# Performance work log

Hardware: AMD Instinct MI355X
Metric: run time of the kernel (lower is better)

## Reference

```python
import jax, jax.numpy as jnp
import numpy as np

N_NODES = 100000
N_EDGES = 3200000
IN_DIM = 256
HID = 16
OUT = 10


def setup_inputs() -> dict:
    key = jax.random.key(0)
    k1, k2, k3, k4, k5, k6 = jax.random.split(key, 6)
    x = jax.random.normal(k1, (N_NODES, IN_DIM), dtype=jnp.float32)
    edge_index = jax.random.randint(k2, (2, N_EDGES), 0, N_NODES, dtype=jnp.int64)
    # Glorot-style init for GCN weights, zeros for bias (PyG defaults)
    W1 = jax.random.normal(k3, (IN_DIM, HID), dtype=jnp.float32) * (1.0 / np.sqrt(IN_DIM))
    b1 = jnp.zeros((HID,), dtype=jnp.float32)
    W2 = jax.random.normal(k4, (HID, OUT), dtype=jnp.float32) * (1.0 / np.sqrt(HID))
    b2 = jnp.zeros((OUT,), dtype=jnp.float32)
    return {"x": x, "edge_index": edge_index, "W1": W1, "b1": b1, "W2": W2, "b2": b2}


def _gcn_conv(h, src, dst, W, b, num_nodes):
    # GCNConv(normalize=False): out_i = sum_{(j->i) in E} (h_j W) + b
    m = h @ W                                   # [N, F_out] small GEMM
    agg = jax.ops.segment_sum(m[src], dst, num_segments=num_nodes)  # gather+scatter-add
    return agg + b


def reference(x, edge_index, W1, b1, W2, b2):
    src = edge_index[0]  # message source (flow: source_to_target)
    dst = edge_index[1]
    n = x.shape[0]
    h = jax.nn.relu(_gcn_conv(x, src, dst, W1, b1, n))
    # F.dropout with module in eval mode -> identity
    out = _gcn_conv(h, src, dst, W2, b2, n)
    return out
```

## Files before the change

### kernel.cpp

```cpp
#include <hip/hip_runtime.h>
#include <hip/hip_bf16.h>
#include <stdint.h>

#define IN_DIM 256
#define HID 16
#define OUTD 10
#define BKT_SHIFT 8
#define BKT_W 256
#define PART_CH 2048
#define EPT 8

typedef short v8s __attribute__((ext_vector_type(8)));
typedef float v4f __attribute__((ext_vector_type(4)));

__device__ __forceinline__ float bf2f(unsigned short u) {
    return __uint_as_float(((unsigned int)u) << 16);
}
__device__ __forceinline__ unsigned short f2bf(float f) {
    unsigned int u = __float_as_uint(f);
    unsigned int lsb = (u >> 16) & 1u;
    u += 0x7fffu + lsb;
    return (unsigned short)(u >> 16);
}

__device__ __forceinline__ int load_dst(const void* ei, int n_edges, int e, int is64) {
    return is64 ? (int)((const long long*)ei)[(size_t)n_edges + e]
                : ((const int*)ei)[(size_t)n_edges + e];
}
__device__ __forceinline__ int load_src(const void* ei, int n_edges, int e, int is64) {
    return is64 ? (int)((const long long*)ei)[e] : ((const int*)ei)[e];
}

__global__ void setup_w1_kernel(const void* __restrict__ x,
                                const void* __restrict__ W1,
                                const void* __restrict__ ei,
                                int n_nodes, int* __restrict__ flags,
                                int* __restrict__ bucket_cnt, int K,
                                unsigned short* __restrict__ W1split) {
    int b = blockIdx.x, t = threadIdx.x;
    int gid = b * blockDim.x + t;
    for (int i = gid; i < K; i += gridDim.x * blockDim.x) bucket_cnt[i] = 0;

    if (b == 16) {
        if (t < 64) {
            const unsigned short* xs = (const unsigned short*)x;
            const unsigned short* ws = (const unsigned short*)W1;
            bool badx = false, badw = false;
#pragma unroll
            for (int q = 0; q < 4; ++q) {
                float vx = bf2f(xs[t + 64 * q]);
                float vw = bf2f(ws[t + 64 * q]);
                if (!(vx > -1e4f && vx < 1e4f)) badx = true;
                if (!(vw > -1e4f && vw < 1e4f)) badw = true;
            }
            const unsigned long long* e64 = (const unsigned long long*)ei;
            bool big = false;
#pragma unroll
            for (int q = 0; q < 2; ++q)
                if (e64[t + 64 * q] >= (unsigned long long)n_nodes) big = true;
            int xf32 = __any(badx) ? 1 : 0;
            int wf32 = __any(badw) ? 1 : 0;
            int is64 = __any(big) ? 0 : 1;
            if (t == 0) { flags[0] = is64; flags[1] = xf32; flags[2] = wf32; }
        }
        return;
    }

    __shared__ int swf32;
    if (t == 0) swf32 = 0;
    __syncthreads();
    {
        float vw = bf2f(((const unsigned short*)W1)[t]);
        if (!(vw > -1e4f && vw < 1e4f)) swf32 = 1;
    }
    __syncthreads();
    const int wf32 = swf32;

    int i = b * 256 + t;
    float w = wf32 ? ((const float*)W1)[i]
                   : bf2f(((const unsigned short*)W1)[i]);
    unsigned short hi = f2bf(w);
    unsigned short lo = f2bf(w - bf2f(hi));
    int k = i >> 4, n = i & 15;
    int kk = k >> 5, qd = (k >> 3) & 3, j = k & 7;
    int idx = ((kk * 4 + qd) * 16 + n) * 8 + j;
    W1split[idx] = hi;
    W1split[4096 + idx] = lo;
}

__global__ __launch_bounds__(256, 4) void gemm1_bhist_kernel(
        const void* __restrict__ xp_,
        const unsigned short* __restrict__ W1split,
        unsigned short* __restrict__ m1,
        const void* __restrict__ ei,
        int* __restrict__ bucket_cnt,
        int n_nodes, int n_edges, int K,
        const int* __restrict__ flags, int g_gemm) {
    __shared__ int lh[512];
    int t = threadIdx.x;
    if ((int)blockIdx.x >= g_gemm) {
        for (int i = t; i < 512; i += 256) lh[i] = 0;
        __syncthreads();
        int is64 = flags[0];
        int vbid = blockIdx.x - g_gemm;
        int stride = (gridDim.x - g_gemm) * 256;
        for (int e = vbid * 256 + t; e < n_edges; e += stride) {
            int d = load_dst(ei, n_edges, e, is64);
            atomicAdd(&lh[d >> BKT_SHIFT], 1);
        }
        __syncthreads();
        for (int i = t; i < K; i += 256)
            if (lh[i]) atomicAdd(&bucket_cnt[i], lh[i]);
        return;
    }
    const int xf32 = flags[1];
    int lane = t & 63;
    int wave = t >> 6;
    int col  = lane & 15;
    int quad = lane >> 4;
    int n_tiles = (n_nodes + 15) >> 4;
    const unsigned short* Whi = W1split;
    const unsigned short* Wlo = W1split + 4096;

    if (!xf32) {
        const unsigned short* x = (const unsigned short*)xp_;
        for (int tile = blockIdx.x * 4 + wave; tile < n_tiles; tile += g_gemm * 4) {
            int row = tile * 16 + col;
            int r = row < n_nodes ? row : n_nodes - 1;
            const unsigned short* xp = x + (size_t)r * IN_DIM + quad * 8;
            v8s a[8];
#pragma unroll
            for (int kk = 0; kk < 8; ++kk)
                a[kk] = *(const v8s*)(xp + kk * 32);
            v4f acc1 = {0.f, 0.f, 0.f, 0.f};
            v4f acc2 = {0.f, 0.f, 0.f, 0.f};
#pragma unroll
            for (int kk = 0; kk < 8; ++kk) {
                v8s bh = *(const v8s*)&Whi[(kk * 64 + lane) * 8];
                v8s bl = *(const v8s*)&Wlo[(kk * 64 + lane) * 8];
                acc1 = __builtin_amdgcn_mfma_f32_16x16x32_bf16(a[kk], bh, acc1, 0, 0, 0);
                acc2 = __builtin_amdgcn_mfma_f32_16x16x32_bf16(a[kk], bl, acc2, 0, 0, 0);
            }
#pragma unroll
            for (int rg = 0; rg < 4; ++rg) {
                int node = tile * 16 + quad * 4 + rg;
                if (node < n_nodes)
                    m1[(size_t)node * HID + col] = f2bf(acc1[rg] + acc2[rg]);
            }
        }
    } else {
        const float* x = (const float*)xp_;
        for (int tile = blockIdx.x * 4 + wave; tile < n_tiles; tile += g_gemm * 4) {
            int row = tile * 16 + col;
            int r = row < n_nodes ? row : n_nodes - 1;
            const float* xp = x + (size_t)r * IN_DIM + quad * 8;
            float4 u[16];
#pragma unroll
            for (int kk = 0; kk < 8; ++kk) {
                u[2 * kk]     = *(const float4*)(xp + kk * 32);
                u[2 * kk + 1] = *(const float4*)(xp + kk * 32 + 4);
            }
            v4f acc1 = {0.f, 0.f, 0.f, 0.f};
            v4f acc2 = {0.f, 0.f, 0.f, 0.f};
#pragma unroll
            for (int kk = 0; kk < 8; ++kk) {
                float uv[8] = {u[2 * kk].x,     u[2 * kk].y,
                               u[2 * kk].z,     u[2 * kk].w,
                               u[2 * kk + 1].x, u[2 * kk + 1].y,
                               u[2 * kk + 1].z, u[2 * kk + 1].w};
                v8s ahi, alo;
#pragma unroll
                for (int j = 0; j < 8; ++j) {
                    unsigned short hi = f2bf(uv[j]);
                    unsigned short lo = f2bf(uv[j] - bf2f(hi));
                    ahi[j] = (short)hi; alo[j] = (short)lo;
                }
                v8s bh = *(const v8s*)&Whi[(kk * 64 + lane) * 8];
                v8s bl = *(const v8s*)&Wlo[(kk * 64 + lane) * 8];
                acc1 = __builtin_amdgcn_mfma_f32_16x16x32_bf16(ahi, bh, acc1, 0, 0, 0);
                acc2 = __builtin_amdgcn_mfma_f32_16x16x32_bf16(ahi, bl, acc2, 0, 0, 0);
                acc2 = __builtin_amdgcn_mfma_f32_16x16x32_bf16(alo, bh, acc2, 0, 0, 0);
            }
#pragma unroll
            for (int rg = 0; rg < 4; ++rg) {
                int node = tile * 16 + quad * 4 + rg;
                if (node < n_nodes)
                    m1[(size_t)node * HID + col] = f2bf(acc1[rg] + acc2[rg]);
            }
        }
    }
}

__global__ void bscan_kernel(const int* __restrict__ bucket_cnt, int K,
                             int* __restrict__ bucket_off, int* __restrict__ bcur,
                             int* __restrict__ row_off, int n_nodes, int n_edges) {
    __shared__ int ts[256];
    int t = threadIdx.x;
    const int KP = (K + 255) / 256;
    int base = t * KP;
    int local[8];
    int s = 0;
    for (int q = 0; q < KP; ++q) {
        int idx = base + q;
        int v = (idx < K) ? bucket_cnt[idx] : 0;
        local[q] = v; s += v;
    }
    ts[t] = s;
    __syncthreads();
    for (int off = 1; off < 256; off <<= 1) {
        int v = (t >= off) ? ts[t - off] : 0;
        __syncthreads();
        ts[t] += v;
        __syncthreads();
    }
    int ex = ts[t] - s;
    for (int q = 0; q < KP; ++q) {
        int idx = base + q;
        if (idx < K) { bucket_off[idx] = ex; bcur[idx] = ex; }
        ex += local[q];
    }
    if (t == 255) bucket_off[K] = ex;
    if (t == 0) row_off[n_nodes] = n_edges;
}

__global__ void part_kernel(const void* __restrict__ ei, int n_edges,
                            int* __restrict__ bcur, unsigned int* __restrict__ pairs,
                            const int* __restrict__ flags, int K) {
    __shared__ int lh[512];
    __shared__ int gdelta[512];
    __shared__ int ts[256];
    __shared__ unsigned int spairs[PART_CH];
    __shared__ unsigned short sbkt[PART_CH];
    int begin = blockIdx.x * PART_CH;
    int is64 = flags[0];
    int t = threadIdx.x;
    lh[t] = 0; lh[t + 256] = 0;

    int dloc[EPT];
#pragma unroll
    for (int i = 0; i < EPT; ++i) {
        int e = begin + i * 256 + t;
        dloc[i] = (e < n_edges) ? load_dst(ei, n_edges, e, is64) : -1;
    }
    __syncthreads();
#pragma unroll
    for (int i = 0; i < EPT; ++i)
        if (dloc[i] >= 0) atomicAdd(&lh[dloc[i] >> BKT_SHIFT], 1);
    __syncthreads();

    int c0 = lh[2 * t], c1 = lh[2 * t + 1];
    int s = c0 + c1;
    ts[t] = s;
    __syncthreads();
    for (int off = 1; off < 256; off <<= 1) {
        int v = (t >= off) ? ts[t - off] : 0;
        __syncthreads();
        ts[t] += v;
        __syncthreads();
    }
    int ex = ts[t] - s;
    if (c0 > 0) gdelta[2 * t]     = atomicAdd(&bcur[2 * t], c0) - ex;
    if (c1 > 0) gdelta[2 * t + 1] = atomicAdd(&bcur[2 * t + 1], c1) - (ex + c0);
    __syncthreads();
    lh[2 * t] = ex; lh[2 * t + 1] = ex + c0;
    __syncthreads();

#pragma unroll
    for (int i = 0; i < EPT; ++i) {
        int e = begin + i * 256 + t;
        if (dloc[i] >= 0) {
            int srcv = load_src(ei, n_edges, e, is64);
            int b = dloc[i] >> BKT_SHIFT;
            int lpos = atomicAdd(&lh[b], 1);
            spairs[lpos] = ((unsigned)srcv << 8) | ((unsigned)dloc[i] & (BKT_W - 1));
            sbkt[lpos] = (unsigned short)b;
        }
    }
    __syncthreads();

    int total = n_edges - begin; if (total > PART_CH) total = PART_CH;
    for (int j = t; j < total; j += 256)
        pairs[gdelta[sbkt[j]] + j] = spairs[j];
}

__global__ void csr_kernel(const unsigned int* __restrict__ pairs,
                           const int* __restrict__ bucket_off,
                           int* __restrict__ row_off, int* __restrict__ csr_src,
                           int n_nodes) {
    __shared__ int deg[BKT_W];
    __shared__ int cur[BKT_W];
    __shared__ int ts[BKT_W];
    int blk = blockIdx.x;
    int nbase = blk << BKT_SHIFT;
    int NL = n_nodes - nbase; if (NL > BKT_W) NL = BKT_W;
    int beg = bucket_off[blk], end = bucket_off[blk + 1];
    int t = threadIdx.x;
    if (t < BKT_W) deg[t] = 0;
    __syncthreads();
    for (int k = beg + t; k < end; k += blockDim.x)
        atomicAdd(&deg[pairs[k] & (BKT_W - 1)], 1);
    __syncthreads();
    if (t < BKT_W) ts[t] = deg[t];
    __syncthreads();
    for (int off = 1; off < BKT_W; off <<= 1) {
        int v = 0;
        if (t < BKT_W && t >= off) v = ts[t - off];
        __syncthreads();
        if (t < BKT_W) ts[t] += v;
        __syncthreads();
    }
    if (t < BKT_W) {
        int ex = beg + ts[t] - deg[t];
        cur[t] = ex;
        if (t < NL) row_off[nbase + t] = ex;
    }
    __syncthreads();
    for (int k = beg + t; k < end; k += blockDim.x) {
        unsigned int p = pairs[k];
        int pos = atomicAdd(&cur[p & (BKT_W - 1)], 1);
        csr_src[pos] = (int)(p >> 8);
    }
}

__device__ __forceinline__ v4f gather_bf16(const unsigned short* __restrict__ src,
                                           const int* __restrict__ csr_src,
                                           int beg, int end, int q) {
    float a0 = 0.f, a1 = 0.f, a2 = 0.f, a3 = 0.f;
    int k = beg;
    for (; k + 16 <= end; k += 16) {
        uint2 v[16];
#pragma unroll
        for (int u = 0; u < 16; ++u) {
            int s = csr_src[k + u];
            v[u] = *(const uint2*)(src + (size_t)s * HID + q * 4);
        }
#pragma unroll
        for (int u = 0; u < 16; ++u) {
            a0 += bf2f((unsigned short)(v[u].x));
            a1 += bf2f((unsigned short)(v[u].x >> 16));
            a2 += bf2f((unsigned short)(v[u].y));
            a3 += bf2f((unsigned short)(v[u].y >> 16));
        }
    }
    for (; k + 4 <= end; k += 4) {
        uint2 v[4];
#pragma unroll
        for (int u = 0; u < 4; ++u) {
            int s = csr_src[k + u];
            v[u] = *(const uint2*)(src + (size_t)s * HID + q * 4);
        }
#pragma unroll
        for (int u = 0; u < 4; ++u) {
            a0 += bf2f((unsigned short)(v[u].x));
            a1 += bf2f((unsigned short)(v[u].x >> 16));
            a2 += bf2f((unsigned short)(v[u].y));
            a3 += bf2f((unsigned short)(v[u].y >> 16));
        }
    }
    for (; k < end; ++k) {
        int s = csr_src[k];
        uint2 v = *(const uint2*)(src + (size_t)s * HID + q * 4);
        a0 += bf2f((unsigned short)(v.x));
        a1 += bf2f((unsigned short)(v.x >> 16));
        a2 += bf2f((unsigned short)(v.y));
        a3 += bf2f((unsigned short)(v.y >> 16));
    }
    v4f r = {a0, a1, a2, a3};
    return r;
}

__global__ void agg1_kernel(const unsigned short* __restrict__ m1,
                            const int* __restrict__ row_off,
                            const int* __restrict__ csr_src,
                            const void* __restrict__ b1p,
                            unsigned short* __restrict__ h, int n_nodes,
                            const int* __restrict__ flags) {
    int t = blockIdx.x * blockDim.x + threadIdx.x;
    int node = t >> 2;
    if (node >= n_nodes) return;
    int q = t & 3;
    const int wf32 = flags[2];
    v4f a = gather_bf16(m1, csr_src, row_off[node], row_off[node + 1], q);
    float b0, b1v, b2v, b3;
    if (wf32) {
        const float* b = (const float*)b1p + q * 4;
        b0 = b[0]; b1v = b[1]; b2v = b[2]; b3 = b[3];
    } else {
        const unsigned short* b = (const unsigned short*)b1p + q * 4;
        b0 = bf2f(b[0]); b1v = bf2f(b[1]); b2v = bf2f(b[2]); b3 = bf2f(b[3]);
    }
    float r0 = fmaxf(a[0] + b0, 0.f);
    float r1 = fmaxf(a[1] + b1v, 0.f);
    float r2 = fmaxf(a[2] + b2v, 0.f);
    float r3 = fmaxf(a[3] + b3, 0.f);
    uint2 packed;
    packed.x = (unsigned int)f2bf(r0) | ((unsigned int)f2bf(r1) << 16);
    packed.y = (unsigned int)f2bf(r2) | ((unsigned int)f2bf(r3) << 16);
    *(uint2*)(h + (size_t)node * HID + q * 4) = packed;
}

__global__ void agg2_out_kernel(const unsigned short* __restrict__ h,
                                const int* __restrict__ row_off,
                                const int* __restrict__ csr_src,
                                const void* __restrict__ W2p,
                                const void* __restrict__ b2p,
                                void* __restrict__ out, int n_nodes,
                                const int* __restrict__ flags) {
    __shared__ float Ws[HID * OUTD];
    __shared__ float bs[OUTD];
    const int xf32 = flags[1], wf32 = flags[2];
    if (threadIdx.x < HID * OUTD)
        Ws[threadIdx.x] = wf32 ? ((const float*)W2p)[threadIdx.x]
                               : bf2f(((const unsigned short*)W2p)[threadIdx.x]);
    if (threadIdx.x < OUTD)
        bs[threadIdx.x] = wf32 ? ((const float*)b2p)[threadIdx.x]
                               : bf2f(((const unsigned short*)b2p)[threadIdx.x]);
    __syncthreads();

    int t = blockIdx.x * blockDim.x + threadIdx.x;
    int node = t >> 2;
    if (node >= n_nodes) return;
    int q = t & 3;
    v4f a = gather_bf16(h, csr_src, row_off[node], row_off[node + 1], q);

    float o[OUTD];
#pragma unroll
    for (int od = 0; od < OUTD; ++od) {
        float s = 0.f;
#pragma unroll
        for (int j = 0; j < 4; ++j)
            s = fmaf(a[j], Ws[(q * 4 + j) * OUTD + od], s);
        o[od] = s;
    }
#pragma unroll
    for (int od = 0; od < OUTD; ++od) {
        o[od] += __shfl_xor(o[od], 1);
        o[od] += __shfl_xor(o[od], 2);
        o[od] += bs[od];
    }

    if (xf32) {
        float2* po = (float2*)((float*)out + (size_t)node * OUTD);
        if (q == 0) {
            po[0] = make_float2(o[0], o[1]);
            po[1] = make_float2(o[2], o[3]);
        } else if (q == 1) {
            po[2] = make_float2(o[4], o[5]);
            po[3] = make_float2(o[6], o[7]);
        } else if (q == 2) {
            po[4] = make_float2(o[8], o[9]);
        }
    } else {
        unsigned int* po = (unsigned int*)((unsigned short*)out + (size_t)node * OUTD);
        if (q == 0) {
            po[0] = (unsigned int)f2bf(o[0]) | ((unsigned int)f2bf(o[1]) << 16);
            po[1] = (unsigned int)f2bf(o[2]) | ((unsigned int)f2bf(o[3]) << 16);
        } else if (q == 1) {
            po[2] = (unsigned int)f2bf(o[4]) | ((unsigned int)f2bf(o[5]) << 16);
            po[3] = (unsigned int)f2bf(o[6]) | ((unsigned int)f2bf(o[7]) << 16);
        } else if (q == 2) {
            po[4] = (unsigned int)f2bf(o[8]) | ((unsigned int)f2bf(o[9]) << 16);
        }
    }
}

__global__ void sentinel_kernel(float* __restrict__ out) {
    if (blockIdx.x == 0 && threadIdx.x < 16) out[threadIdx.x] = 123456.0f;
}

extern "C" void kernel_launch(void* const* d_in, const int* in_sizes, int n_in,
                              void* d_out, int out_size, void* d_ws, size_t ws_size,
                              hipStream_t stream) {
    const void* x  = d_in[0];
    const void* ei = d_in[1];
    const void* W1 = d_in[2];
    const void* b1 = d_in[3];
    const void* W2 = d_in[4];
    const void* b2 = d_in[5];

    const int n_nodes = in_sizes[0] / IN_DIM;
    const int n_edges = in_sizes[1] / 2;
    const int K = (n_nodes + BKT_W - 1) / BKT_W;

    char* p = (char*)d_ws;
    auto align = [](size_t v) { return (v + 255) & ~(size_t)255; };
    size_t off = 0;
    int* flags      = (int*)(p + off); off = align(off + 256);
    unsigned short* w1split = (unsigned short*)(p + off); off = align(off + 8192 * 2);
    int* bucket_cnt = (int*)(p + off); off = align(off + (size_t)K * 4);
    int* bucket_off = (int*)(p + off); off = align(off + ((size_t)K + 1) * 4);
    int* bcur       = (int*)(p + off); off = align(off + (size_t)K * 4);
    int* row_off    = (int*)(p + off); off = align(off + ((size_t)n_nodes + 1) * 4);
    int* csr_src    = (int*)(p + off); off = align(off + (size_t)n_edges * 4);
    unsigned int* pairs = (unsigned int*)(p + off); off = align(off + (size_t)n_edges * 4);
    unsigned short* m1 = (unsigned short*)(p + off); off = align(off + (size_t)n_nodes * HID * 2);
    unsigned short* h  = (unsigned short*)(p + off); off = align(off + (size_t)n_nodes * HID * 2);

    if (ws_size < off) {
        sentinel_kernel<<<1, 64, 0, stream>>>((float*)d_out);
        return;
    }

    const int n_tiles16 = (n_nodes + 15) >> 4;
    const int g_gemm = (n_tiles16 + 3) / 4;
    const int g_hist = 512;

    setup_w1_kernel<<<17, 256, 0, stream>>>(x, W1, ei, n_nodes, flags,
                                            bucket_cnt, K, w1split);

    gemm1_bhist_kernel<<<g_gemm + g_hist, 256, 0, stream>>>(
        x, w1split, m1, ei, bucket_cnt, n_nodes, n_edges, K, flags, g_gemm);

    bscan_kernel<<<1, 256, 0, stream>>>(bucket_cnt, K, bucket_off, bcur,
                                        row_off, n_nodes, n_edges);

    part_kernel<<<(n_edges + PART_CH - 1) / PART_CH, 256, 0, stream>>>(
        ei, n_edges, bcur, pairs, flags, K);

    csr_kernel<<<K, 512, 0, stream>>>(pairs, bucket_off, row_off, csr_src, n_nodes);

    {
        long long threads = (long long)n_nodes * 4;
        agg1_kernel<<<(int)((threads + 255) / 256), 256, 0, stream>>>(
            m1, row_off, csr_src, b1, h, n_nodes, flags);
    }

    {
        long long threads = (long long)n_nodes * 4;
        agg2_out_kernel<<<(int)((threads + 255) / 256), 256, 0, stream>>>(
            h, row_off, csr_src, W2, b2, d_out, n_nodes, flags);
    }
}
```

Measured before the change: 348.9 us.

## Regroup kernels: fuse partition with GEMM1 and CSR build with layer-1 aggregation

The launch schedule is reorganized. The bucket histogram now runs alongside the W1 split setup, the edge partition runs in the same grid as the first-layer GEMM, and the CSR build is fused with layer-1 aggregation, which reads source indices from shared memory. This removes one kernel launch plus the global round trip of csr_src before agg1, and it overlaps the GEMM with partitioning. In exchange, each partition block handles twice as many edges, shared memory per CSR block grows, and buckets larger than the shared capacity fall back to global reads.

```diff
diff --git a/kernel.cpp b/kernel.cpp
--- a/kernel.cpp
+++ b/kernel.cpp
@@ -7,8 +7,10 @@
 #define OUTD 10
 #define BKT_SHIFT 8
 #define BKT_W 256
-#define PART_CH 2048
-#define EPT 8
+#define PART_CH 4096
+#define EPT 16
+#define G_HIST 512
+#define SSRC_CAP 8704
 
 typedef short v8s __attribute__((ext_vector_type(8)));
 typedef float v4f __attribute__((ext_vector_type(4)));
@@ -31,16 +33,42 @@
     return is64 ? (int)((const long long*)ei)[e] : ((const int*)ei)[e];
 }
 
-__global__ void setup_w1_kernel(const void* __restrict__ x,
-                                const void* __restrict__ W1,
-                                const void* __restrict__ ei,
-                                int n_nodes, int* __restrict__ flags,
-                                int* __restrict__ bucket_cnt, int K,
-                                unsigned short* __restrict__ W1split) {
+__global__ void zero_kernel(int* __restrict__ bucket_cnt, int K) {
+    for (int i = threadIdx.x; i < K; i += blockDim.x) bucket_cnt[i] = 0;
+}
+
+__global__ void setup_bhist_kernel(const void* __restrict__ x,
+                                   const void* __restrict__ W1,
+                                   const void* __restrict__ ei,
+                                   int n_nodes, int n_edges,
+                                   int* __restrict__ flags,
+                                   int* __restrict__ bucket_cnt, int K,
+                                   unsigned short* __restrict__ W1split) {
+    __shared__ int lh[512];
+    __shared__ int sflag;
     int b = blockIdx.x, t = threadIdx.x;
-    int gid = b * blockDim.x + t;
-    for (int i = gid; i < K; i += gridDim.x * blockDim.x) bucket_cnt[i] = 0;
-
+
+    if (b < 16) {
+        if (t == 0) sflag = 0;
+        __syncthreads();
+        {
+            float vw = bf2f(((const unsigned short*)W1)[t]);
+            if (!(vw > -1e4f && vw < 1e4f)) sflag = 1;
+        }
+        __syncthreads();
+        const int wf32 = sflag;
+        int i = b * 256 + t;
+        float w = wf32 ? ((const float*)W1)[i]
+                       : bf2f(((const unsigned short*)W1)[i]);
+        unsigned short hi = f2bf(w);
+        unsigned short lo = f2bf(w - bf2f(hi));
+        int k = i >> 4, n = i & 15;
+        int kk = k >> 5, qd = (k >> 3) & 3, j = k & 7;
+        int idx = ((kk * 4 + qd) * 16 + n) * 8 + j;
+        W1split[idx] = hi;
+        W1split[4096 + idx] = lo;
+        return;
+    }
     if (b == 16) {
         if (t < 64) {
             const unsigned short* xs = (const unsigned short*)x;
@@ -66,129 +94,25 @@
         return;
     }
 
-    __shared__ int swf32;
-    if (t == 0) swf32 = 0;
+    if (t == 0) sflag = 1;
     __syncthreads();
     {
-        float vw = bf2f(((const unsigned short*)W1)[t]);
-        if (!(vw > -1e4f && vw < 1e4f)) swf32 = 1;
-    }
-    __syncthreads();
-    const int wf32 = swf32;
-
-    int i = b * 256 + t;
-    float w = wf32 ? ((const float*)W1)[i]
-                   : bf2f(((const unsigned short*)W1)[i]);
-    unsigned short hi = f2bf(w);
-    unsigned short lo = f2bf(w - bf2f(hi));
-    int k = i >> 4, n = i & 15;
-    int kk = k >> 5, qd = (k >> 3) & 3, j = k & 7;
-    int idx = ((kk * 4 + qd) * 16 + n) * 8 + j;
-    W1split[idx] = hi;
-    W1split[4096 + idx] = lo;
-}
-
-__global__ __launch_bounds__(256, 4) void gemm1_bhist_kernel(
-        const void* __restrict__ xp_,
-        const unsigned short* __restrict__ W1split,
-        unsigned short* __restrict__ m1,
-        const void* __restrict__ ei,
-        int* __restrict__ bucket_cnt,
-        int n_nodes, int n_edges, int K,
-        const int* __restrict__ flags, int g_gemm) {
-    __shared__ int lh[512];
-    int t = threadIdx.x;
-    if ((int)blockIdx.x >= g_gemm) {
-        for (int i = t; i < 512; i += 256) lh[i] = 0;
-        __syncthreads();
-        int is64 = flags[0];
-        int vbid = blockIdx.x - g_gemm;
-        int stride = (gridDim.x - g_gemm) * 256;
-        for (int e = vbid * 256 + t; e < n_edges; e += stride) {
-            int d = load_dst(ei, n_edges, e, is64);
-            atomicAdd(&lh[d >> BKT_SHIFT], 1);
-        }
-        __syncthreads();
-        for (int i = t; i < K; i += 256)
-            if (lh[i]) atomicAdd(&bucket_cnt[i], lh[i]);
-        return;
-    }
-    const int xf32 = flags[1];
-    int lane = t & 63;
-    int wave = t >> 6;
-    int col  = lane & 15;
-    int quad = lane >> 4;
-    int n_tiles = (n_nodes + 15) >> 4;
-    const unsigned short* Whi = W1split;
-    const unsigned short* Wlo = W1split + 4096;
-
-    if (!xf32) {
-        const unsigned short* x = (const unsigned short*)xp_;
-        for (int tile = blockIdx.x * 4 + wave; tile < n_tiles; tile += g_gemm * 4) {
-            int row = tile * 16 + col;
-            int r = row < n_nodes ? row : n_nodes - 1;
-            const unsigned short* xp = x + (size_t)r * IN_DIM + quad * 8;
-            v8s a[8];
-#pragma unroll
-            for (int kk = 0; kk < 8; ++kk)
-                a[kk] = *(const v8s*)(xp + kk * 32);
-            v4f acc1 = {0.f, 0.f, 0.f, 0.f};
-            v4f acc2 = {0.f, 0.f, 0.f, 0.f};
-#pragma unroll
-            for (int kk = 0; kk < 8; ++kk) {
-                v8s bh = *(const v8s*)&Whi[(kk * 64 + lane) * 8];
-                v8s bl = *(const v8s*)&Wlo[(kk * 64 + lane) * 8];
-                acc1 = __builtin_amdgcn_mfma_f32_16x16x32_bf16(a[kk], bh, acc1, 0, 0, 0);
-                acc2 = __builtin_amdgcn_mfma_f32_16x16x32_bf16(a[kk], bl, acc2, 0, 0, 0);
-            }
-#pragma unroll
-            for (int rg = 0; rg < 4; ++rg) {
-                int node = tile * 16 + quad * 4 + rg;
-                if (node < n_nodes)
-                    m1[(size_t)node * HID + col] = f2bf(acc1[rg] + acc2[rg]);
-            }
-        }
-    } else {
-        const float* x = (const float*)xp_;
-        for (int tile = blockIdx.x * 4 + wave; tile < n_tiles; tile += g_gemm * 4) {
-            int row = tile * 16 + col;
-            int r = row < n_nodes ? row : n_nodes - 1;
-            const float* xp = x + (size_t)r * IN_DIM + quad * 8;
-            float4 u[16];
-#pragma unroll
-            for (int kk = 0; kk < 8; ++kk) {
-                u[2 * kk]     = *(const float4*)(xp + kk * 32);
-                u[2 * kk + 1] = *(const float4*)(xp + kk * 32 + 4);
-            }
-            v4f acc1 = {0.f, 0.f, 0.f, 0.f};
-            v4f acc2 = {0.f, 0.f, 0.f, 0.f};
-#pragma unroll
-            for (int kk = 0; kk < 8; ++kk) {
-                float uv[8] = {u[2 * kk].x,     u[2 * kk].y,
-                               u[2 * kk].z,     u[2 * kk].w,
-                               u[2 * kk + 1].x, u[2 * kk + 1].y,
-                               u[2 * kk + 1].z, u[2 * kk + 1].w};
-                v8s ahi, alo;
-#pragma unroll
-                for (int j = 0; j < 8; ++j) {
-                    unsigned short hi = f2bf(uv[j]);
-                    unsigned short lo = f2bf(uv[j] - bf2f(hi));
-                    ahi[j] = (short)hi; alo[j] = (short)lo;
-                }
-                v8s bh = *(const v8s*)&Whi[(kk * 64 + lane) * 8];
-                v8s bl = *(const v8s*)&Wlo[(kk * 64 + lane) * 8];
-                acc1 = __builtin_amdgcn_mfma_f32_16x16x32_bf16(ahi, bh, acc1, 0, 0, 0);
-                acc2 = __builtin_amdgcn_mfma_f32_16x16x32_bf16(ahi, bl, acc2, 0, 0, 0);
-                acc2 = __builtin_amdgcn_mfma_f32_16x16x32_bf16(alo, bh, acc2, 0, 0, 0);
-            }
-#pragma unroll
-            for (int rg = 0; rg < 4; ++rg) {
-                int node = tile * 16 + quad * 4 + rg;
-                if (node < n_nodes)
-                    m1[(size_t)node * HID + col] = f2bf(acc1[rg] + acc2[rg]);
-            }
-        }
-    }
+        const unsigned long long* e64 = (const unsigned long long*)ei;
+        if (t < 128 && e64[t] >= (unsigned long long)n_nodes) sflag = 0;
+    }
+    __syncthreads();
+    const int is64 = sflag;
+    for (int i = t; i < 512; i += 256) lh[i] = 0;
+    __syncthreads();
+    int vbid = b - 17;
+    int stride = G_HIST * 256;
+    for (int e = vbid * 256 + t; e < n_edges; e += stride) {
+        int d = load_dst(ei, n_edges, e, is64);
+        atomicAdd(&lh[d >> BKT_SHIFT], 1);
+    }
+    __syncthreads();
+    for (int i = t; i < K; i += 256)
+        if (lh[i]) atomicAdd(&bucket_cnt[i], lh[i]);
 }
 
 __global__ void bscan_kernel(const int* __restrict__ bucket_cnt, int K,
@@ -223,70 +147,162 @@
     if (t == 0) row_off[n_nodes] = n_edges;
 }
 
-__global__ void part_kernel(const void* __restrict__ ei, int n_edges,
-                            int* __restrict__ bcur, unsigned int* __restrict__ pairs,
-                            const int* __restrict__ flags, int K) {
+__global__ __launch_bounds__(256, 4) void part_gemm1_kernel(
+        const void* __restrict__ ei, int n_edges,
+        int* __restrict__ bcur, unsigned int* __restrict__ pairs,
+        const void* __restrict__ xp_,
+        const unsigned short* __restrict__ W1split,
+        unsigned short* __restrict__ m1, int n_nodes,
+        const int* __restrict__ flags, int K, int g_part) {
     __shared__ int lh[512];
     __shared__ int gdelta[512];
     __shared__ int ts[256];
     __shared__ unsigned int spairs[PART_CH];
     __shared__ unsigned short sbkt[PART_CH];
-    int begin = blockIdx.x * PART_CH;
-    int is64 = flags[0];
     int t = threadIdx.x;
-    lh[t] = 0; lh[t + 256] = 0;
-
-    int dloc[EPT];
-#pragma unroll
-    for (int i = 0; i < EPT; ++i) {
-        int e = begin + i * 256 + t;
-        dloc[i] = (e < n_edges) ? load_dst(ei, n_edges, e, is64) : -1;
-    }
-    __syncthreads();
-#pragma unroll
-    for (int i = 0; i < EPT; ++i)
-        if (dloc[i] >= 0) atomicAdd(&lh[dloc[i] >> BKT_SHIFT], 1);
-    __syncthreads();
-
-    int c0 = lh[2 * t], c1 = lh[2 * t + 1];
-    int s = c0 + c1;
-    ts[t] = s;
-    __syncthreads();
-    for (int off = 1; off < 256; off <<= 1) {
-        int v = (t >= off) ? ts[t - off] : 0;
-        __syncthreads();
-        ts[t] += v;
-        __syncthreads();
-    }
-    int ex = ts[t] - s;
-    if (c0 > 0) gdelta[2 * t]     = atomicAdd(&bcur[2 * t], c0) - ex;
-    if (c1 > 0) gdelta[2 * t + 1] = atomicAdd(&bcur[2 * t + 1], c1) - (ex + c0);
-    __syncthreads();
-    lh[2 * t] = ex; lh[2 * t + 1] = ex + c0;
-    __syncthreads();
-
-#pragma unroll
-    for (int i = 0; i < EPT; ++i) {
-        int e = begin + i * 256 + t;
-        if (dloc[i] >= 0) {
-            int srcv = load_src(ei, n_edges, e, is64);
-            int b = dloc[i] >> BKT_SHIFT;
-            int lpos = atomicAdd(&lh[b], 1);
-            spairs[lpos] = ((unsigned)srcv << 8) | ((unsigned)dloc[i] & (BKT_W - 1));
-            sbkt[lpos] = (unsigned short)b;
-        }
-    }
-    __syncthreads();
-
-    int total = n_edges - begin; if (total > PART_CH) total = PART_CH;
-    for (int j = t; j < total; j += 256)
-        pairs[gdelta[sbkt[j]] + j] = spairs[j];
-}
-
-__global__ void csr_kernel(const unsigned int* __restrict__ pairs,
-                           const int* __restrict__ bucket_off,
-                           int* __restrict__ row_off, int* __restrict__ csr_src,
-                           int n_nodes) {
+
+    if ((int)blockIdx.x < g_part) {
+        int begin = blockIdx.x * PART_CH;
+        int is64 = flags[0];
+        lh[t] = 0; lh[t + 256] = 0;
+
+        int dloc[EPT];
+#pragma unroll
+        for (int i = 0; i < EPT; ++i) {
+            int e = begin + i * 256 + t;
+            dloc[i] = (e < n_edges) ? load_dst(ei, n_edges, e, is64) : -1;
+        }
+        __syncthreads();
+#pragma unroll
+        for (int i = 0; i < EPT; ++i)
+            if (dloc[i] >= 0) atomicAdd(&lh[dloc[i] >> BKT_SHIFT], 1);
+        __syncthreads();
+
+        int c0 = lh[2 * t], c1 = lh[2 * t + 1];
+        int s = c0 + c1;
+        ts[t] = s;
+        __syncthreads();
+        for (int off = 1; off < 256; off <<= 1) {
+            int v = (t >= off) ? ts[t - off] : 0;
+            __syncthreads();
+            ts[t] += v;
+            __syncthreads();
+        }
+        int ex = ts[t] - s;
+        if (c0 > 0) gdelta[2 * t]     = atomicAdd(&bcur[2 * t], c0) - ex;
+        if (c1 > 0) gdelta[2 * t + 1] = atomicAdd(&bcur[2 * t + 1], c1) - (ex + c0);
+        __syncthreads();
+        lh[2 * t] = ex; lh[2 * t + 1] = ex + c0;
+        __syncthreads();
+
+#pragma unroll
+        for (int i = 0; i < EPT; ++i) {
+            int e = begin + i * 256 + t;
+            if (dloc[i] >= 0) {
+                int srcv = load_src(ei, n_edges, e, is64);
+                int bb = dloc[i] >> BKT_SHIFT;
+                int lpos = atomicAdd(&lh[bb], 1);
+                spairs[lpos] = ((unsigned)srcv << 8) | ((unsigned)dloc[i] & (BKT_W - 1));
+                sbkt[lpos] = (unsigned short)bb;
+            }
+        }
+        __syncthreads();
+
+        int total = n_edges - begin; if (total > PART_CH) total = PART_CH;
+        for (int j = t; j < total; j += 256)
+            pairs[gdelta[sbkt[j]] + j] = spairs[j];
+        return;
+    }
+
+    const int xf32 = flags[1];
+    int vb = blockIdx.x - g_part;
+    int g_gemm = gridDim.x - g_part;
+    int lane = t & 63;
+    int wave = t >> 6;
+    int col  = lane & 15;
+    int quad = lane >> 4;
+    int n_tiles = (n_nodes + 15) >> 4;
+    const unsigned short* Whi = W1split;
+    const unsigned short* Wlo = W1split + 4096;
+
+    if (!xf32) {
+        const unsigned short* x = (const unsigned short*)xp_;
+        for (int tile = vb * 4 + wave; tile < n_tiles; tile += g_gemm * 4) {
+            int row = tile * 16 + col;
+            int r = row < n_nodes ? row : n_nodes - 1;
+            const unsigned short* xp = x + (size_t)r * IN_DIM + quad * 8;
+            v8s a[8];
+#pragma unroll
+            for (int kk = 0; kk < 8; ++kk)
+                a[kk] = *(const v8s*)(xp + kk * 32);
+            v4f acc1 = {0.f, 0.f, 0.f, 0.f};
+            v4f acc2 = {0.f, 0.f, 0.f, 0.f};
+#pragma unroll
+            for (int kk = 0; kk < 8; ++kk) {
+                v8s bh = *(const v8s*)&Whi[(kk * 64 + lane) * 8];
+                v8s bl = *(const v8s*)&Wlo[(kk * 64 + lane) * 8];
+                acc1 = __builtin_amdgcn_mfma_f32_16x16x32_bf16(a[kk], bh, acc1, 0, 0, 0);
+                acc2 = __builtin_amdgcn_mfma_f32_16x16x32_bf16(a[kk], bl, acc2, 0, 0, 0);
+            }
+#pragma unroll
+            for (int rg = 0; rg < 4; ++rg) {
+                int node = tile * 16 + quad * 4 + rg;
+                if (node < n_nodes)
+                    m1[(size_t)node * HID + col] = f2bf(acc1[rg] + acc2[rg]);
+            }
+        }
+    } else {
+        const float* x = (const float*)xp_;
+        for (int tile = vb * 4 + wave; tile < n_tiles; tile += g_gemm * 4) {
+            int row = tile * 16 + col;
+            int r = row < n_nodes ? row : n_nodes - 1;
+            const float* xp = x + (size_t)r * IN_DIM + quad * 8;
+            float4 u[16];
+#pragma unroll
+            for (int kk = 0; kk < 8; ++kk) {
+                u[2 * kk]     = *(const float4*)(xp + kk * 32);
+                u[2 * kk + 1] = *(const float4*)(xp + kk * 32 + 4);
+            }
+            v4f acc1 = {0.f, 0.f, 0.f, 0.f};
+            v4f acc2 = {0.f, 0.f, 0.f, 0.f};
+#pragma unroll
+            for (int kk = 0; kk < 8; ++kk) {
+                float uv[8] = {u[2 * kk].x,     u[2 * kk].y,
+                               u[2 * kk].z,     u[2 * kk].w,
+                               u[2 * kk + 1].x, u[2 * kk + 1].y,
+                               u[2 * kk + 1].z, u[2 * kk + 1].w};
+                v8s ahi, alo;
+#pragma unroll
+                for (int j = 0; j < 8; ++j) {
+                    unsigned short hi = f2bf(uv[j]);
+                    unsigned short lo = f2bf(uv[j] - bf2f(hi));
+                    ahi[j] = (short)hi; alo[j] = (short)lo;
+                }
+                v8s bh = *(const v8s*)&Whi[(kk * 64 + lane) * 8];
+                v8s bl = *(const v8s*)&Wlo[(kk * 64 + lane) * 8];
+                acc1 = __builtin_amdgcn_mfma_f32_16x16x32_bf16(ahi, bh, acc1, 0, 0, 0);
+                acc2 = __builtin_amdgcn_mfma_f32_16x16x32_bf16(ahi, bl, acc2, 0, 0, 0);
+                acc2 = __builtin_amdgcn_mfma_f32_16x16x32_bf16(alo, bh, acc2, 0, 0, 0);
+            }
+#pragma unroll
+            for (int rg = 0; rg < 4; ++rg) {
+                int node = tile * 16 + quad * 4 + rg;
+                if (node < n_nodes)
+                    m1[(size_t)node * HID + col] = f2bf(acc1[rg] + acc2[rg]);
+            }
+        }
+    }
+}
+
+__global__ __launch_bounds__(512) void csr_agg1_kernel(
+        const unsigned int* __restrict__ pairs,
+        const int* __restrict__ bucket_off,
+        const unsigned short* __restrict__ m1,
+        const void* __restrict__ b1p,
+        int* __restrict__ row_off, int* __restrict__ csr_src,
+        unsigned short* __restrict__ h,
+        int n_nodes, const int* __restrict__ flags) {
+    __shared__ unsigned int ssrc[SSRC_CAP];
     __shared__ int deg[BKT_W];
     __shared__ int cur[BKT_W];
     __shared__ int ts[BKT_W];
@@ -295,9 +311,10 @@
     int NL = n_nodes - nbase; if (NL > BKT_W) NL = BKT_W;
     int beg = bucket_off[blk], end = bucket_off[blk + 1];
     int t = threadIdx.x;
+
     if (t < BKT_W) deg[t] = 0;
     __syncthreads();
-    for (int k = beg + t; k < end; k += blockDim.x)
+    for (int k = beg + t; k < end; k += 512)
         atomicAdd(&deg[pairs[k] & (BKT_W - 1)], 1);
     __syncthreads();
     if (t < BKT_W) ts[t] = deg[t];
@@ -310,15 +327,70 @@
         __syncthreads();
     }
     if (t < BKT_W) {
-        int ex = beg + ts[t] - deg[t];
-        cur[t] = ex;
-        if (t < NL) row_off[nbase + t] = ex;
-    }
-    __syncthreads();
-    for (int k = beg + t; k < end; k += blockDim.x) {
-        unsigned int p = pairs[k];
-        int pos = atomicAdd(&cur[p & (BKT_W - 1)], 1);
-        csr_src[pos] = (int)(p >> 8);
+        int exl = ts[t] - deg[t];
+        cur[t] = exl;
+        if (t < NL) row_off[nbase + t] = beg + exl;
+    }
+    __syncthreads();
+    for (int k = beg + t; k < end; k += 512) {
+        unsigned int pr = pairs[k];
+        int dl = pr & (BKT_W - 1);
+        int pos = atomicAdd(&cur[dl], 1);
+        int src = (int)(pr >> 8);
+        csr_src[beg + pos] = src;
+        if (pos < SSRC_CAP) ssrc[pos] = (unsigned)src;
+    }
+    __syncthreads();
+
+    const int wf32 = flags[2];
+    int q = t & 3, grp = t >> 2;
+    float b0, b1v, b2v, b3;
+    if (wf32) {
+        const float* b = (const float*)b1p + q * 4;
+        b0 = b[0]; b1v = b[1]; b2v = b[2]; b3 = b[3];
+    } else {
+        const unsigned short* b = (const unsigned short*)b1p + q * 4;
+        b0 = bf2f(b[0]); b1v = bf2f(b[1]); b2v = bf2f(b[2]); b3 = bf2f(b[3]);
+    }
+    for (int nl = grp; nl < NL; nl += 128) {
+        int sL = ts[nl] - deg[nl];
+        int eL = ts[nl];
+        float a0 = 0.f, a1 = 0.f, a2 = 0.f, a3 = 0.f;
+        int k = sL;
+        for (; k + 8 <= eL; k += 8) {
+            int sidx[8];
+            uint2 v[8];
+#pragma unroll
+            for (int u = 0; u < 8; ++u)
+                sidx[u] = (k + u < SSRC_CAP) ? (int)ssrc[k + u]
+                                             : csr_src[beg + k + u];
+#pragma unroll
+            for (int u = 0; u < 8; ++u)
+                v[u] = *(const uint2*)(m1 + (size_t)sidx[u] * HID + q * 4);
+#pragma unroll
+            for (int u = 0; u < 8; ++u) {
+                a0 += bf2f((unsigned short)(v[u].x));
+                a1 += bf2f((unsigned short)(v[u].x >> 16));
+                a2 += bf2f((unsigned short)(v[u].y));
+                a3 += bf2f((unsigned short)(v[u].y >> 16));
+            }
+        }
+        for (; k < eL; ++k) {
+            int s = (k < SSRC_CAP) ? (int)ssrc[k] : csr_src[beg + k];
+            uint2 v = *(const uint2*)(m1 + (size_t)s * HID + q * 4);
+            a0 += bf2f((unsigned short)(v.x));
+            a1 += bf2f((unsigned short)(v.x >> 16));
+            a2 += bf2f((unsigned short)(v.y));
+            a3 += bf2f((unsigned short)(v.y >> 16));
+        }
+        float r0 = fmaxf(a0 + b0, 0.f);
+        float r1 = fmaxf(a1 + b1v, 0.f);
+        float r2 = fmaxf(a2 + b2v, 0.f);
+        float r3 = fmaxf(a3 + b3, 0.f);
+        uint2 packed;
+        packed.x = (unsigned int)f2bf(r0) | ((unsigned int)f2bf(r1) << 16);
+        packed.y = (unsigned int)f2bf(r2) | ((unsigned int)f2bf(r3) << 16);
+        *(uint2*)(h + (size_t)(nbase + nl) * HID + q * 4) = packed;
     }
 }
 
@@ -367,36 +439,6 @@
     }
     v4f r = {a0, a1, a2, a3};
     return r;
-}
-
-__global__ void agg1_kernel(const unsigned short* __restrict__ m1,
-                            const int* __restrict__ row_off,
-                            const int* __restrict__ csr_src,
-                            const void* __restrict__ b1p,
-                            unsigned short* __restrict__ h, int n_nodes,
-                            const int* __restrict__ flags) {
-    int t = blockIdx.x * blockDim.x + threadIdx.x;
-    int node = t >> 2;
-    if (node >= n_nodes) return;
-    int q = t & 3;
-    const int wf32 = flags[2];
-    v4f a = gather_bf16(m1, csr_src, row_off[node], row_off[node + 1], q);
-    float b0, b1v, b2v, b3;
-    if (wf32) {
-        const float* b = (const float*)b1p + q * 4;
-        b0 = b[0]; b1v = b[1]; b2v = b[2]; b3 = b[3];
-    } else {
-        const unsigned short* b = (const unsigned short*)b1p + q * 4;
-        b0 = bf2f(b[0]); b1v = bf2f(b[1]); b2v = bf2f(b[2]); b3 = bf2f(b[3]);
-    }
-    float r0 = fmaxf(a[0] + b0, 0.f);
-    float r1 = fmaxf(a[1] + b1v, 0.f);
-    float r2 = fmaxf(a[2] + b2v, 0.f);
-    float r3 = fmaxf(a[3] + b3, 0.f);
-    uint2 packed;
-    packed.x = (unsigned int)f2bf(r0) | ((unsigned int)f2bf(r1) << 16);
-    packed.y = (unsigned int)f2bf(r2) | ((unsigned int)f2bf(r3) << 16);
-    *(uint2*)(h + (size_t)node * HID + q * 4) = packed;
 }
 
 __global__ void agg2_out_kernel(const unsigned short* __restrict__ h,
@@ -503,27 +545,21 @@
 
     const int n_tiles16 = (n_nodes + 15) >> 4;
     const int g_gemm = (n_tiles16 + 3) / 4;
-    const int g_hist = 512;
-
-    setup_w1_kernel<<<17, 256, 0, stream>>>(x, W1, ei, n_nodes, flags,
-                                            bucket_cnt, K, w1split);
-
-    gemm1_bhist_kernel<<<g_gemm + g_hist, 256, 0, stream>>>(
-        x, w1split, m1, ei, bucket_cnt, n_nodes, n_edges, K, flags, g_gemm);
+    const int g_part = (n_edges + PART_CH - 1) / PART_CH;
+
+    zero_kernel<<<1, 256, 0, stream>>>(bucket_cnt, K);
+
+    setup_bhist_kernel<<<17 + G_HIST, 256, 0, stream>>>(
+        x, W1, ei, n_nodes, n_edges, flags, bucket_cnt, K, w1split);
 
     bscan_kernel<<<1, 256, 0, stream>>>(bucket_cnt, K, bucket_off, bcur,
                                         row_off, n_nodes, n_edges);
 
-    part_kernel<<<(n_edges + PART_CH - 1) / PART_CH, 256, 0, stream>>>(
-        ei, n_edges, bcur, pairs, flags, K);
-
-    csr_kernel<<<K, 512, 0, stream>>>(pairs, bucket_off, row_off, csr_src, n_nodes);
-
-    {
-        long long threads = (long long)n_nodes * 4;
-        agg1_kernel<<<(int)((threads + 255) / 256), 256, 0, stream>>>(
-            m1, row_off, csr_src, b1, h, n_nodes, flags);
-    }
+    part_gemm1_kernel<<<g_part + g_gemm, 256, 0, stream>>>(
+        ei, n_edges, bcur, pairs, x, w1split, m1, n_nodes, flags, K, g_part);
+
+    csr_agg1_kernel<<<K, 512, 0, stream>>>(pairs, bucket_off, m1, b1,
+                                           row_off, csr_src, h, n_nodes, flags);
 
     {
         long long threads = (long long)n_nodes * 4;
```

New measurement: 311.3 us. -10.8%, faster.
